# Performance work log

Measured on AMD Instinct MI355X. Metric: run time of the kernel, lower is better.

## Reference

```python
import jax, jax.numpy as jnp
import numpy as np

N_SOURCE = 100000
N_TARGET = 4096
DEG = 800                      # edges per target (uniform)
N_EDGES = N_TARGET * DEG       # 3,276,800
SOURCE_DIM = 512
EMBED_DIM = 32
TARGET_DIM = 16


def setup_inputs() -> dict:
    key = jax.random.key(0)
    k1, k2, k3, k4, k5 = jax.random.split(key, 5)
    source_feat = jax.random.normal(k1, (N_SOURCE, SOURCE_DIM), dtype=jnp.float32)
    embed = jax.random.normal(k2, (SOURCE_DIM, EMBED_DIM), dtype=jnp.float32)
    weight = jax.random.normal(k3, (EMBED_DIM, TARGET_DIM), dtype=jnp.float32)
    # edges sorted by target; range_list[i] = [start, end) of target i's edge block
    src = jax.random.randint(k4, (N_EDGES,), 0, N_SOURCE, dtype=jnp.int64)
    tgt = jnp.repeat(jnp.arange(N_TARGET, dtype=jnp.int64), DEG)
    edge_index = jnp.stack([src, tgt], axis=0)
    starts = jnp.arange(N_TARGET, dtype=jnp.int64) * DEG
    range_list = jnp.stack([starts, starts + DEG], axis=1)
    x_norm = jax.random.uniform(k5, (N_SOURCE,), dtype=jnp.float32) + 0.5
    return {"source_feat": source_feat, "embed": embed, "weight": weight,
            "edge_index": edge_index, "range_list": range_list, "x_norm": x_norm}


def reference(source_feat, embed, weight, edge_index, range_list, x_norm):
    # dense embed GEMM + row normalization
    x = jnp.matmul(source_feat, embed)              # [N_SOURCE, EMBED_DIM]
    x = x / x_norm[:, None]
    # hierarchical conv: gather source rows, mean-aggregate per target segment
    tmp = x[edge_index[0]]                           # [N_EDGES, EMBED_DIM]
    agg = jax.ops.segment_sum(tmp, edge_index[1], num_segments=N_TARGET)
    deg = (range_list[:, 1] - range_list[:, 0]).astype(x.dtype)
    out = agg / jnp.maximum(deg, 1.0)[:, None]       # [N_TARGET, EMBED_DIM]
    out = jnp.matmul(out, weight)                    # [N_TARGET, TARGET_DIM]
    return out
```

## Files before the change

### kernel.cpp

```cpp
#include <hip/hip_runtime.h>
#include <hip/hip_bf16.h>

#define N_SOURCE   100000
#define N_TARGET   4096
#define SOURCE_DIM 512
#define EMBED_DIM  32
#define TARGET_DIM 16
#define NTILES     ((N_SOURCE + 15) / 16)

typedef __attribute__((ext_vector_type(8))) short short8;
typedef __attribute__((ext_vector_type(4))) float f32x4;

static __device__ __forceinline__ ushort f2bf(float f) {
    __hip_bfloat16 h = __float2bfloat16(f);
    return *(ushort*)&h;
}

__global__ __launch_bounds__(256)
void k_embed_weight(const float* __restrict__ embed,
                    const float* __restrict__ weight,
                    ushort* __restrict__ Mt) {
    __shared__ float wlds[EMBED_DIM * TARGET_DIM];
    int tid = threadIdx.x;
    for (int i = tid; i < EMBED_DIM * TARGET_DIM; i += 256)
        wlds[i] = weight[i];
    __syncthreads();

    int idx = blockIdx.x * 256 + tid;
    if (idx < SOURCE_DIM * TARGET_DIM) {
        int k = idx >> 4;
        int o = idx & 15;
        float s = 0.f;
        #pragma unroll
        for (int j = 0; j < EMBED_DIM; ++j)
            s += embed[k * EMBED_DIM + j] * wlds[j * TARGET_DIM + o];
        Mt[o * SOURCE_DIM + k] = f2bf(s);
    }
}

__global__ __launch_bounds__(256, 2)
void k_gemm_y(const float*  __restrict__ A,
              const float*  __restrict__ xnorm,
              const ushort* __restrict__ Mt,
              ushort*       __restrict__ y) {
    extern __shared__ ushort smem[];
    ushort* Bl  = smem;
    int tid  = threadIdx.x;
    int wave = tid >> 6;
    int lane = tid & 63;
    ushort* AlW = smem + 8192 + wave * 8192;

    #pragma unroll
    for (int i = 0; i < 4; ++i) {
        int c  = tid + 256 * i;
        int nn = c & 15;
        int kg = c >> 4;
        int kk = kg >> 2;
        int gg = kg & 3;
        *(uint4*)&Bl[c * 8] =
            *(const uint4*)(Mt + nn * SOURCE_DIM + kk * 32 + gg * 8);
    }

    int tile  = blockIdx.x * 4 + wave;
    int tilec = tile < NTILES ? tile : NTILES - 1;
    int row0  = tilec * 16;

    int laneConst = ((lane >> 3) << 10) | (((lane >> 1) & 3) << 8) | ((lane & 1) << 3);
    int xl        = ((laneConst >> 8) & 7);

    #pragma unroll
    for (int j = 0; j < 32; ++j) {
        int r = j >> 1, h = j & 1;
        f32x4 v = *(const f32x4*)(A + (size_t)(row0 + r) * SOURCE_DIM
                                    + h * 256 + lane * 4);
        uint d0 = (uint)f2bf(v[0]) | ((uint)f2bf(v[1]) << 16);
        uint d1 = (uint)f2bf(v[2]) | ((uint)f2bf(v[3]) << 16);
        int phys = (h << 13) + (laneConst & ~0xF8) + (laneConst & 0x700)
                 + (laneConst & 0x7C00)
                 ;
        phys = laneConst + (h << 13) + ((r ^ xl) << 4);
        *(uint2*)((char*)AlW + phys) = make_uint2(d0, d1);
    }

    __syncthreads();

    if (tile < NTILES) {
        int n = lane & 15;
        int g = lane >> 4;
        const ushort* Bll = Bl + lane * 8;

        f32x4 acc = {0.f, 0.f, 0.f, 0.f};
        #pragma unroll
        for (int kk = 0; kk < 16; ++kk) {
            int xr = (4 * kk + (lane >> 4)) & 7;
            const short8 af = *(const short8*)
                ((char*)AlW + kk * 1024 + ((lane ^ xr) << 4));
            const short8 bf = *(const short8*)(Bll + kk * 512);
            acc = __builtin_amdgcn_mfma_f32_16x16x32_bf16(af, bf, acc, 0, 0, 0);
        }

        int m0 = g * 4;
        float4 xn = *(const float4*)(xnorm + row0 + m0);
        const float xr4[4] = {xn.x, xn.y, xn.z, xn.w};
        #pragma unroll
        for (int r = 0; r < 4; ++r)
            y[(size_t)(row0 + m0 + r) * TARGET_DIM + n] = f2bf(acc[r] / xr4[r]);
    }
}

__global__ __launch_bounds__(256)
void k_gather_mean(const ushort* __restrict__ y,
                   const int*    __restrict__ src,
                   const int*    __restrict__ rl,
                   float* __restrict__ out) {
    int t     = blockIdx.x;
    int tid   = threadIdx.x;
    int start = rl[2 * t];
    int end   = rl[2 * t + 1];

    int slot = tid >> 1;
    int sub  = tid & 1;

    float a[8];
    #pragma unroll
    for (int i = 0; i < 8; ++i) a[i] = 0.f;

    for (int base = start + slot * 4; base < end; base += 512) {
        int rem = end - base;
        int id[4];
        if (rem >= 4) {
            int4 qd = *(const int4*)(src + base);
            id[0] = qd.x; id[1] = qd.y; id[2] = qd.z; id[3] = qd.w;
        } else {
            #pragma unroll
            for (int j = 0; j < 4; ++j) id[j] = (j < rem) ? src[base + j] : 0;
        }
        #pragma unroll
        for (int j = 0; j < 4; ++j) {
            if (j < rem) {
                uint4 v = *(const uint4*)(y + (size_t)id[j] * TARGET_DIM + sub * 8);
                const uint w[4] = {v.x, v.y, v.z, v.w};
                #pragma unroll
                for (int i = 0; i < 4; ++i) {
                    uint lo = w[i] << 16;
                    uint hiw = w[i] & 0xffff0000u;
                    a[2 * i]     += *(float*)&lo;
                    a[2 * i + 1] += *(float*)&hiw;
                }
            }
        }
    }

    #pragma unroll
    for (int m = 2; m <= 32; m <<= 1) {
        #pragma unroll
        for (int i = 0; i < 8; ++i) a[i] += __shfl_xor(a[i], m);
    }

    __shared__ float red[4][16];
    int wid  = tid >> 6;
    int lane = tid & 63;
    if (lane < 2) {
        #pragma unroll
        for (int i = 0; i < 8; ++i) red[wid][lane * 8 + i] = a[i];
    }
    __syncthreads();

    if (tid < TARGET_DIM) {
        float s = red[0][tid] + red[1][tid] + red[2][tid] + red[3][tid];
        float deg = (float)(end - start);
        deg = deg > 1.f ? deg : 1.f;
        out[t * TARGET_DIM + tid] = s / deg;
    }
}

extern "C" void kernel_launch(void* const* d_in, const int* in_sizes, int n_in,
                              void* d_out, int out_size, void* d_ws, size_t ws_size,
                              hipStream_t stream) {
    const float* source_feat = (const float*)d_in[0];
    const float* embed       = (const float*)d_in[1];
    const float* weight      = (const float*)d_in[2];
    const int*   edge_src    = (const int*)d_in[3];
    const int*   range_list  = (const int*)d_in[4];
    const float* x_norm      = (const float*)d_in[5];

    float*  out = (float*)d_out;
    ushort* Mt  = (ushort*)d_ws;
    ushort* y   = (ushort*)((char*)d_ws + 16384);

    k_embed_weight<<<32, 256, 0, stream>>>(embed, weight, Mt);

    int nblk = (NTILES + 3) / 4;
    k_gemm_y<<<nblk, 256, 81920, stream>>>(source_feat, x_norm, Mt, y);

    k_gather_mean<<<N_TARGET, 256, 0, stream>>>(y, edge_src, range_list, out);
}
```

Baseline: 61.50 us.

## Split GEMM K into halves to cut LDS and overlap loads with MFMA

The y-GEMM kernel now stages only half of each 16-row A tile (256 of 512 columns) in LDS per wave. It issues global loads for the second half before running the first half's MFMAs, then overwrites the same LDS buffer and runs the rest. This halves per-wave LDS (dynamic shared memory goes from 80KB to 48KB) and raises launch bounds to 3 blocks per CU, aiming for more occupancy and more memory requests in flight on this bandwidth-bound pass. The trade-off is higher register pressure from holding 16 float4 prefetches per lane, which could cause spills.

```diff
diff --git a/kernel.cpp b/kernel.cpp
--- a/kernel.cpp
+++ b/kernel.cpp
@@ -38,7 +38,7 @@
     }
 }
 
-__global__ __launch_bounds__(256, 2)
+__global__ __launch_bounds__(256, 3)
 void k_gemm_y(const float*  __restrict__ A,
               const float*  __restrict__ xnorm,
               const ushort* __restrict__ Mt,
@@ -48,7 +48,7 @@
     int tid  = threadIdx.x;
     int wave = tid >> 6;
     int lane = tid & 63;
-    ushort* AlW = smem + 8192 + wave * 8192;
+    ushort* AlW = smem + 8192 + wave * 4096;
 
     #pragma unroll
     for (int i = 0; i < 4; ++i) {
@@ -66,39 +66,60 @@
     int row0  = tilec * 16;
 
     int laneConst = ((lane >> 3) << 10) | (((lane >> 1) & 3) << 8) | ((lane & 1) << 3);
-    int xl        = ((laneConst >> 8) & 7);
-
-    #pragma unroll
-    for (int j = 0; j < 32; ++j) {
-        int r = j >> 1, h = j & 1;
-        f32x4 v = *(const f32x4*)(A + (size_t)(row0 + r) * SOURCE_DIM
-                                    + h * 256 + lane * 4);
-        uint d0 = (uint)f2bf(v[0]) | ((uint)f2bf(v[1]) << 16);
-        uint d1 = (uint)f2bf(v[2]) | ((uint)f2bf(v[3]) << 16);
-        int phys = (h << 13) + (laneConst & ~0xF8) + (laneConst & 0x700)
-                 + (laneConst & 0x7C00)
-                 ;
-        phys = laneConst + (h << 13) + ((r ^ xl) << 4);
-        *(uint2*)((char*)AlW + phys) = make_uint2(d0, d1);
+    int xl        = (laneConst >> 8) & 7;
+
+    f32x4 v0[16];
+    #pragma unroll
+    for (int r = 0; r < 16; ++r)
+        v0[r] = *(const f32x4*)(A + (size_t)(row0 + r) * SOURCE_DIM + lane * 4);
+
+    #pragma unroll
+    for (int r = 0; r < 16; ++r) {
+        uint d0 = (uint)f2bf(v0[r][0]) | ((uint)f2bf(v0[r][1]) << 16);
+        uint d1 = (uint)f2bf(v0[r][2]) | ((uint)f2bf(v0[r][3]) << 16);
+        *(uint2*)((char*)AlW + laneConst + ((r ^ xl) << 4)) = make_uint2(d0, d1);
     }
 
     __syncthreads();
 
+    f32x4 v1[16];
+    #pragma unroll
+    for (int r = 0; r < 16; ++r)
+        v1[r] = *(const f32x4*)(A + (size_t)(row0 + r) * SOURCE_DIM + 256 + lane * 4);
+
+    int n = lane & 15;
+    int g = lane >> 4;
+    const ushort* Bll = Bl + lane * 8;
+
+    f32x4 acc = {0.f, 0.f, 0.f, 0.f};
+
+    #pragma unroll
+    for (int kk = 0; kk < 8; ++kk) {
+        int xr = (4 * kk + (lane >> 4)) & 7;
+        const short8 af = *(const short8*)
+            ((char*)AlW + kk * 1024 + ((lane ^ xr) << 4));
+        const short8 bf = *(const short8*)(Bll + kk * 512);
+        acc = __builtin_amdgcn_mfma_f32_16x16x32_bf16(af, bf, acc, 0, 0, 0);
+    }
+
+    #pragma unroll
+    for (int r = 0; r < 16; ++r) {
+        uint d0 = (uint)f2bf(v1[r][0]) | ((uint)f2bf(v1[r][1]) << 16);
+        uint d1 = (uint)f2bf(v1[r][2]) | ((uint)f2bf(v1[r][3]) << 16);
+        *(uint2*)((char*)AlW + laneConst + ((r ^ xl) << 4)) = make_uint2(d0, d1);
+    }
+
+    #pragma unroll
+    for (int kk = 8; kk < 16; ++kk) {
+        int kl = kk - 8;
+        int xr = (4 * kl + (lane >> 4)) & 7;
+        const short8 af = *(const short8*)
+            ((char*)AlW + kl * 1024 + ((lane ^ xr) << 4));
+        const short8 bf = *(const short8*)(Bll + kk * 512);
+        acc = __builtin_amdgcn_mfma_f32_16x16x32_bf16(af, bf, acc, 0, 0, 0);
+    }
+
     if (tile < NTILES) {
-        int n = lane & 15;
-        int g = lane >> 4;
-        const ushort* Bll = Bl + lane * 8;
-
-        f32x4 acc = {0.f, 0.f, 0.f, 0.f};
-        #pragma unroll
-        for (int kk = 0; kk < 16; ++kk) {
-            int xr = (4 * kk + (lane >> 4)) & 7;
-            const short8 af = *(const short8*)
-                ((char*)AlW + kk * 1024 + ((lane ^ xr) << 4));
-            const short8 bf = *(const short8*)(Bll + kk * 512);
-            acc = __builtin_amdgcn_mfma_f32_16x16x32_bf16(af, bf, acc, 0, 0, 0);
-        }
-
         int m0 = g * 4;
         float4 xn = *(const float4*)(xnorm + row0 + m0);
         const float xr4[4] = {xn.x, xn.y, xn.z, xn.w};
@@ -191,7 +212,7 @@
     k_embed_weight<<<32, 256, 0, stream>>>(embed, weight, Mt);
 
     int nblk = (NTILES + 3) / 4;
-    k_gemm_y<<<nblk, 256, 81920, stream>>>(source_feat, x_norm, Mt, y);
+    k_gemm_y<<<nblk, 256, 49152, stream>>>(source_feat, x_norm, Mt, y);
 
     k_gather_mean<<<N_TARGET, 256, 0, stream>>>(y, edge_src, range_list, out);
 }
```

Result: slower. 63.13 us (+2.7%).
